# Performance work log

Measured on AMD Instinct MI355X. Metric: run time of the kernel, lower is better.

The kernel has to match this reference:

```python
import jax, jax.numpy as jnp
import numpy as np

N_NODES = 100000
N_EDGES = 600000
N_GRAPHS = 2000
H = 128
L = 3
EPS = 1e-5


def layer_norm(x, g, b):
    m = jnp.mean(x, axis=-1, keepdims=True)
    v = jnp.mean((x - m) ** 2, axis=-1, keepdims=True)
    return (x - m) / jnp.sqrt(v + EPS) * g + b


def setup_inputs() -> dict:
    key = jax.random.key(0)
    ks = jax.random.split(key, 32)
    s = 0.05
    d = {}
    d['atom_features'] = jax.random.normal(ks[0], (N_NODES, 4), jnp.float32)
    d['edge_index'] = jax.random.randint(ks[1], (2, N_EDGES), 0, N_NODES, jnp.int32)
    d['edge_attr'] = jax.random.uniform(ks[2], (N_EDGES, 1), jnp.float32)
    d['batch'] = jnp.sort(jax.random.randint(ks[3], (N_NODES,), 0, N_GRAPHS, jnp.int32))
    # atom encoder
    d['enc_w'] = jax.random.normal(ks[4], (4, H)) * s
    d['enc_b'] = jnp.zeros((H,))
    d['enc_ln_g'] = jnp.ones((H,))
    d['enc_ln_b'] = jnp.zeros((H,))
    # stacked per-layer MPNN params (L layers)
    d['msg_w1'] = jax.random.normal(ks[5], (L, 2 * H + 1, 2 * H)) * s
    d['msg_b1'] = jnp.zeros((L, 2 * H))
    d['msg_w2'] = jax.random.normal(ks[6], (L, 2 * H, H)) * s
    d['msg_b2'] = jnp.zeros((L, H))
    d['gru_wih'] = jax.random.normal(ks[7], (L, 3 * H, H)) * s
    d['gru_whh'] = jax.random.normal(ks[8], (L, 3 * H, H)) * s
    d['gru_bih'] = jnp.zeros((L, 3 * H))
    d['gru_bhh'] = jnp.zeros((L, 3 * H))
    d['ln_g'] = jnp.ones((L, H))
    d['ln_b'] = jnp.zeros((L, H))
    # readout MLP (dropout is eval-mode identity)
    d['ro_w1'] = jax.random.normal(ks[9], (2 * H, H)) * s
    d['ro_b1'] = jnp.zeros((H,))
    d['ro_w2'] = jax.random.normal(ks[10], (H, H // 2)) * s
    d['ro_b2'] = jnp.zeros((H // 2,))
    d['ro_w3'] = jax.random.normal(ks[11], (H // 2, 113)) * s
    d['ro_b3'] = jnp.zeros((113,))
    return d


def _forward(atom_features, edge_attr, enc_w, enc_b, enc_ln_g, enc_ln_b,
             msg_w1, msg_b1, msg_w2, msg_b2, gru_wih, gru_whh, gru_bih, gru_bhh,
             ln_g, ln_b, ro_w1, ro_b1, ro_w2, ro_b2, ro_w3, ro_b3,
             edge_index, batch):
    n = atom_features.shape[0]
    x = layer_norm(jax.nn.relu(atom_features @ enc_w + enc_b), enc_ln_g, enc_ln_b)
    src, dst = edge_index[0], edge_index[1]
    for l in range(L):
        # gather-concat-MLP messages: [E, 2H+1] -> [E, 2H] -> [E, H]
        m = jnp.concatenate([x[src], x[dst], edge_attr], axis=-1)
        m = jax.nn.relu(m @ msg_w1[l] + msg_b1[l]) @ msg_w2[l] + msg_b2[l]
        aggr = jax.ops.segment_sum(m, dst, num_segments=n)  # index_add
        # GRUCell(input=aggr, hidden=x)
        gi = aggr @ gru_wih[l].T + gru_bih[l]
        gh = x @ gru_whh[l].T + gru_bhh[l]
        i_r, i_z, i_n = jnp.split(gi, 3, axis=-1)
        h_r, h_z, h_n = jnp.split(gh, 3, axis=-1)
        r = jax.nn.sigmoid(i_r + h_r)
        z = jax.nn.sigmoid(i_z + h_z)
        nn_ = jnp.tanh(i_n + r * h_n)
        x_new = (1.0 - z) * nn_ + z * x
        x = layer_norm(x + x_new, ln_g[l], ln_b[l])
    # per-graph mean+max pooling
    ones = jnp.ones((n,), x.dtype)
    counts = jax.ops.segment_sum(ones, batch, num_segments=N_GRAPHS)
    mean_pool = jax.ops.segment_sum(x, batch, num_segments=N_GRAPHS) / jnp.maximum(counts, 1.0)[:, None]
    max_pool = jax.ops.segment_max(x, batch, num_segments=N_GRAPHS)
    g = jnp.concatenate([mean_pool, max_pool], axis=-1)  # [B, 2H]
    h1 = jax.nn.relu(g @ ro_w1 + ro_b1)
    h2 = jax.nn.relu(h1 @ ro_w2 + ro_b2)
    return h2 @ ro_w3 + ro_b3  # [B, 113]


def reference(atom_features, edge_index, edge_attr, batch, enc_w, enc_b, enc_ln_g, enc_ln_b,
              msg_w1, msg_b1, msg_w2, msg_b2, gru_wih, gru_whh, gru_bih, gru_bhh,
              ln_g, ln_b, ro_w1, ro_b1, ro_w2, ro_b2, ro_w3, ro_b3):
    return _forward(atom_features, edge_attr, enc_w, enc_b, enc_ln_g, enc_ln_b,
                    msg_w1, msg_b1, msg_w2, msg_b2, gru_wih, gru_whh, gru_bih, gru_bhh,
                    ln_g, ln_b, ro_w1, ro_b1, ro_w2, ro_b2, ro_w3, ro_b3,
                    edge_index, batch)
```

## Files before the change

kernel.cpp:

```cpp
#include <hip/hip_runtime.h>
#include <hip/hip_bf16.h>
#include <math.h>

#define NN 100000
#define NE_TOT 600000
#define NG 2000
#define HD 128
#define NL 3
#define LN_EPS 1e-5f

typedef __attribute__((ext_vector_type(8))) short short8;
typedef __attribute__((ext_vector_type(4))) float f32x4;

__device__ __forceinline__ unsigned short f2bf(float f){
  union { float f; unsigned int u; } x; x.f = f;
  unsigned int r = (x.u + 0x7FFFu + ((x.u >> 16) & 1u)) >> 16;
  return (unsigned short)r;
}
__device__ __forceinline__ float bf2f(unsigned short u){
  union { unsigned int i; float f; } x; x.i = ((unsigned int)u) << 16; return x.f;
}

__device__ __forceinline__ float wave_sum64(float v){
  #pragma unroll
  for (int o = 32; o > 0; o >>= 1) v += __shfl_xor(v, o, 64);
  return v;
}

__global__ __launch_bounds__(256) void k_zero4(float4* p, int n4){
  int i = blockIdx.x * 256 + threadIdx.x;
  if (i < n4) p[i] = make_float4(0.f, 0.f, 0.f, 0.f);
}

__global__ __launch_bounds__(256) void k_hist(const int* __restrict__ ei, int* __restrict__ cnt){
  int e = blockIdx.x * 256 + threadIdx.x;
  if (e < NE_TOT) atomicAdd(&cnt[ei[NE_TOT + e]], 1);
}

__global__ __launch_bounds__(1024) void k_scan1(const int* __restrict__ cnt,
                                                int* __restrict__ loc,
                                                int* __restrict__ bsum){
  __shared__ int w_s[16];
  int t = threadIdx.x, lane = t & 63, wv = t >> 6;
  int g = blockIdx.x * 1024 + t;
  int v = (g < NN) ? cnt[g] : 0;
  int s = v;
  #pragma unroll
  for (int o = 1; o < 64; o <<= 1){
    int u = __shfl_up(s, o, 64);
    if (lane >= o) s += u;
  }
  if (lane == 63) w_s[wv] = s;
  __syncthreads();
  if (t == 0){
    int run = 0;
    #pragma unroll
    for (int i = 0; i < 16; ++i){ int c = w_s[i]; w_s[i] = run; run += c; }
    bsum[blockIdx.x] = run;
  }
  __syncthreads();
  if (g < NN) loc[g] = s - v + w_s[wv];
}

__global__ __launch_bounds__(128) void k_scan2(const int* __restrict__ bsum,
                                               int* __restrict__ bscan){
  __shared__ int w0_s;
  int t = threadIdx.x, lane = t & 63, wv = t >> 6;
  int v = (t < 98) ? bsum[t] : 0;
  int s = v;
  #pragma unroll
  for (int o = 1; o < 64; o <<= 1){
    int u = __shfl_up(s, o, 64);
    if (lane >= o) s += u;
  }
  if (wv == 0 && lane == 63) w0_s = s;
  __syncthreads();
  if (wv == 1) s += w0_s;
  if (t < 98) bscan[t] = s - v;
}

__global__ __launch_bounds__(1024) void k_scan3(const int* __restrict__ loc,
                                                const int* __restrict__ bscan,
                                                int* __restrict__ cur){
  int g = blockIdx.x * 1024 + threadIdx.x;
  if (g < NN) cur[g] = loc[g] + bscan[blockIdx.x];
}

__global__ __launch_bounds__(256) void k_scatter(const int* __restrict__ ei,
    const float* __restrict__ eattr, int* __restrict__ cur,
    int* __restrict__ srcs, int* __restrict__ dsts, float* __restrict__ attrs){
  int e = blockIdx.x * 256 + threadIdx.x;
  if (e >= NE_TOT) return;
  int d = ei[NE_TOT + e];
  int p = atomicAdd(&cur[d], 1);
  srcs[p] = ei[e];
  dsts[p] = d;
  attrs[p] = eattr[e];
}

#define GW_LPL 102400
#define GW_O2  67584
#define GW_O3  84992
__global__ __launch_bounds__(256) void k_gprep(const float* __restrict__ wih,
                                               const float* __restrict__ whh,
                                               unsigned short* __restrict__ gw){
  int idx = blockIdx.x * 256 + threadIdx.x;
  if (idx >= 2 * 3 * 384 * 128) return;
  int which = (idx >= 3 * 384 * 128);
  int i = which ? idx - 3 * 384 * 128 : idx;
  int l = i / 49152;
  int r = i - l * 49152;
  int j = r >> 7, k = r & 127;
  float v = which ? whh[i] : wih[i];
  size_t o;
  if (!which){
    o = (j < 256) ? ((size_t)l * GW_LPL + (size_t)j * 264 + k)
                  : ((size_t)l * GW_LPL + GW_O2 + (size_t)(j - 256) * 136 + k);
  } else {
    o = (j < 256) ? ((size_t)l * GW_LPL + (size_t)j * 264 + 128 + k)
                  : ((size_t)l * GW_LPL + GW_O3 + (size_t)(j - 256) * 136 + k);
  }
  gw[o] = f2bf(v);
}

#define W1N_LS (512 * 136)
__global__ __launch_bounds__(256) void k_mprep(const float* __restrict__ w1,
                                               unsigned short* __restrict__ w1n){
  int idx = blockIdx.x * 256 + threadIdx.x;
  if (idx >= 3 * 512 * 128) return;
  int l = idx / (512 * 128);
  int r = idx - l * (512 * 128);
  int j = r >> 7, k = r & 127;
  const float* wl = w1 + (size_t)l * 257 * 256;
  float v = (j < 256) ? wl[k * 256 + j] : wl[(128 + k) * 256 + (j - 256)];
  w1n[(size_t)l * W1N_LS + j * 136 + k] = f2bf(v);
}

#define W2T_LS (128 * 264)
__global__ __launch_bounds__(256) void k_w2prep(const float* __restrict__ w2,
                                                unsigned short* __restrict__ w2T){
  int idx = blockIdx.x * 256 + threadIdx.x;
  if (idx >= 3 * 128 * 256) return;
  int l = idx >> 15;
  int r = idx & 32767;
  int c = r >> 8, k = r & 255;
  w2T[(size_t)l * W2T_LS + c * 264 + k] = f2bf(w2[(size_t)l * 256 * 128 + k * 128 + c]);
}

__global__ __launch_bounds__(256) void k_enc(const float* __restrict__ af,
    const float* __restrict__ w, const float* __restrict__ b,
    const float* __restrict__ lg, const float* __restrict__ lb,
    unsigned short* __restrict__ xbf){
  int wv = threadIdx.x >> 6, lane = threadIdx.x & 63;
  int n = blockIdx.x * 4 + wv;
  float4 a = *reinterpret_cast<const float4*>(af + (size_t)n * 4);
  int c0 = lane, c1 = lane + 64;
  float v0 = fmaf(a.x, w[c0], fmaf(a.y, w[128 + c0], fmaf(a.z, w[256 + c0], fmaf(a.w, w[384 + c0], b[c0]))));
  float v1 = fmaf(a.x, w[c1], fmaf(a.y, w[128 + c1], fmaf(a.z, w[256 + c1], fmaf(a.w, w[384 + c1], b[c1]))));
  v0 = fmaxf(v0, 0.f); v1 = fmaxf(v1, 0.f);
  float m = wave_sum64(v0 + v1) * (1.f / 128.f);
  float d0 = v0 - m, d1 = v1 - m;
  float var = wave_sum64(d0 * d0 + d1 * d1) * (1.f / 128.f);
  float rstd = rsqrtf(var + LN_EPS);
  xbf[(size_t)n * HD + c0] = f2bf(d0 * rstd * lg[c0] + lb[c0]);
  xbf[(size_t)n * HD + c1] = f2bf(d1 * rstd * lg[c1] + lb[c1]);
}

__global__ __launch_bounds__(256, 2) void k_ngemm(const unsigned short* __restrict__ xbf,
    const unsigned short* __restrict__ w1n, const float* __restrict__ b1,
    unsigned short* __restrict__ gsd){
  int tid = threadIdx.x, lane = tid & 63, wv = tid >> 6;
  int r16 = lane & 15, kg = lane >> 4;
  int n = blockIdx.x * 64 + wv * 16 + r16;
  int nc = (n < NN) ? n : NN - 1;
  short8 bfr[4];
  #pragma unroll
  for (int k0 = 0; k0 < 4; ++k0)
    bfr[k0] = *reinterpret_cast<const short8*>(xbf + (size_t)nc * HD + k0 * 32 + kg * 8);
  f32x4 acc[32];
  #pragma unroll
  for (int it = 0; it < 32; ++it) acc[it] = (f32x4){0.f, 0.f, 0.f, 0.f};
  #pragma unroll
  for (int it = 0; it < 32; ++it){
    const unsigned short* ap = w1n + (size_t)(it * 16 + r16) * 136 + kg * 8;
    #pragma unroll
    for (int k0 = 0; k0 < 4; ++k0){
      short8 af = *reinterpret_cast<const short8*>(ap + k0 * 32);
      acc[it] = __builtin_amdgcn_mfma_f32_16x16x32_bf16(af, bfr[k0], acc[it], 0, 0, 0);
    }
  }
  if (n < NN){
    #pragma unroll
    for (int it = 0; it < 32; ++it){
      int c0 = it * 16 + kg * 4;
      ushort4 h;
      float v0 = acc[it][0], v1 = acc[it][1], v2 = acc[it][2], v3 = acc[it][3];
      if (c0 >= 256){
        v0 += b1[c0 - 256]; v1 += b1[c0 - 255]; v2 += b1[c0 - 254]; v3 += b1[c0 - 253];
      }
      h.x = f2bf(v0); h.y = f2bf(v1); h.z = f2bf(v2); h.w = f2bf(v3);
      *reinterpret_cast<ushort4*>(gsd + (size_t)n * 512 + c0) = h;
    }
  }
}

#define EBM 64
__global__ __launch_bounds__(256, 4) void k_msg(const unsigned short* __restrict__ gsd,
    const int* __restrict__ srcs, const int* __restrict__ dsts,
    const float* __restrict__ attrs, const float* __restrict__ w1attr,
    const unsigned short* __restrict__ w2T, const float* __restrict__ b2,
    float* __restrict__ aggr){
  __shared__ __align__(16) unsigned char smem[33280];
  unsigned short* h_s = (unsigned short*)smem;
  float* scr = (float*)smem;
  __shared__ float w1a_s[256];
  __shared__ float b2_s[128];
  __shared__ int   dst_s[EBM];
  __shared__ float attr_s[EBM];
  int tid = threadIdx.x;
  int lane = tid & 63, wv = tid >> 6;
  int r16 = lane & 15, kg = lane >> 4;
  int ebase = blockIdx.x * EBM;

  w1a_s[tid] = w1attr[tid & 255];
  if (tid < 128) b2_s[tid] = b2[tid];
  if (tid < EBM){ dst_s[tid] = dsts[ebase + tid]; attr_s[tid] = attrs[ebase + tid]; }
  __syncthreads();

  {
    int e = tid >> 2, q = tid & 3;
    int sn = srcs[ebase + e];
    int dn = dst_s[e];
    float at = attr_s[e];
    const unsigned short* gp = gsd + (size_t)sn * 512;
    const unsigned short* dp = gsd + (size_t)dn * 512 + 256;
    #pragma unroll
    for (int j8 = 0; j8 < 8; ++j8){
      int colb = j8 * 32 + q * 8;
      short8 gv = *reinterpret_cast<const short8*>(gp + colb);
      short8 dv = *reinterpret_cast<const short8*>(dp + colb);
      unsigned short hh[8];
      #pragma unroll
      for (int i = 0; i < 8; ++i){
        float v = bf2f((unsigned short)gv[i]) + bf2f((unsigned short)dv[i]) + at * w1a_s[colb + i];
        hh[i] = f2bf(fmaxf(v, 0.f));
      }
      int slot = colb >> 3;
      int slotw = (slot & ~7) | ((slot ^ e) & 7);
      *reinterpret_cast<int4*>(&h_s[e * 256 + slotw * 8]) = *reinterpret_cast<int4*>(hh);
    }
  }
  __syncthreads();

  f32x4 acc2[4][2];
  #pragma unroll
  for (int rt = 0; rt < 4; ++rt)
    #pragma unroll
    for (int ct = 0; ct < 2; ++ct)
      acc2[rt][ct] = (f32x4){0.f, 0.f, 0.f, 0.f};
  int cbase2 = wv * 32;
  {
    short8 a[4], bb[2];
    const unsigned short* w2b = w2T + (size_t)(cbase2 + r16) * 264 + kg * 8;
    for (int k0 = 0; k0 < 8; ++k0){
      #pragma unroll
      for (int rt = 0; rt < 4; ++rt){
        int row = rt * 16 + r16;
        int slot = k0 * 4 + kg;
        int slotw = (slot & ~7) | ((slot ^ row) & 7);
        a[rt] = *reinterpret_cast<const short8*>(&h_s[row * 256 + slotw * 8]);
      }
      #pragma unroll
      for (int ct = 0; ct < 2; ++ct)
        bb[ct] = *reinterpret_cast<const short8*>(w2b + ct * 16 * 264 + k0 * 32);
      #pragma unroll
      for (int rt = 0; rt < 4; ++rt)
        #pragma unroll
        for (int ct = 0; ct < 2; ++ct)
          acc2[rt][ct] = __builtin_amdgcn_mfma_f32_16x16x32_bf16(a[rt], bb[ct], acc2[rt][ct], 0, 0, 0);
    }
  }
  __syncthreads();

  #pragma unroll
  for (int ct = 0; ct < 2; ++ct){
    int col = cbase2 + ct * 16 + r16;
    #pragma unroll
    for (int rt = 0; rt < 4; ++rt){
      #pragma unroll
      for (int r = 0; r < 4; ++r){
        int row = rt * 16 + kg * 4 + r;
        scr[row * 130 + col] = acc2[rt][ct][r];
      }
    }
  }
  __syncthreads();

  {
    int c = tid & 127, h = tid >> 7;
    int r0 = h * 32;
    float bias = b2_s[c];
    int pd = dst_s[r0];
    float acc = scr[r0 * 130 + c] + bias;
    #pragma unroll 4
    for (int r = 1; r < 32; ++r){
      int row = r0 + r;
      float v = scr[row * 130 + c] + bias;
      int d = dst_s[row];
      if (d != pd){
        atomicAdd(&aggr[(size_t)pd * HD + c], acc);
        acc = v; pd = d;
      } else {
        acc += v;
      }
    }
    atomicAdd(&aggr[(size_t)pd * HD + c], acc);
  }
}

#define GRB 64
__global__ __launch_bounds__(256, 2) void k_gru(unsigned short* __restrict__ xbf,
    const float* __restrict__ aggr,
    const unsigned short* __restrict__ gw,
    const float* __restrict__ bih, const float* __restrict__ bhh,
    const float* __restrict__ lg, const float* __restrict__ lb){
  __shared__ unsigned short a_s[GRB * 256];
  int tid = threadIdx.x;
  int lane = tid & 63, wv = tid >> 6;
  int r16 = lane & 15, kg = lane >> 4;
  int nbase = blockIdx.x * GRB;

  {
    int row = tid >> 2, qc = (tid & 3) * 32;
    int n = nbase + row; if (n >= NN) n = NN - 1;
    const float* ap = aggr + (size_t)n * HD + qc;
    #pragma unroll
    for (int j = 0; j < 8; ++j){
      float4 v = *reinterpret_cast<const float4*>(ap + j * 4);
      ushort4 h;
      h.x = f2bf(v.x); h.y = f2bf(v.y); h.z = f2bf(v.z); h.w = f2bf(v.w);
      int col = qc + j * 4;
      int slot = col >> 3;
      int slotw = (slot & ~7) | ((slot ^ row) & 7);
      *reinterpret_cast<ushort4*>(&a_s[row * 256 + slotw * 8 + (col & 7)]) = h;
    }
  }
  {
    int row = tid >> 2, q = tid & 3;
    int n = nbase + row; if (n >= NN) n = NN - 1;
    const unsigned short* xp = xbf + (size_t)n * HD + q * 32;
    #pragma unroll
    for (int j = 0; j < 4; ++j){
      int4 v = *reinterpret_cast<const int4*>(xp + j * 8);
      int col = 128 + q * 32 + j * 8;
      int slot = col >> 3;
      int slotw = (slot & ~7) | ((slot ^ row) & 7);
      *reinterpret_cast<int4*>(&a_s[row * 256 + slotw * 8]) = v;
    }
  }
  __syncthreads();

  int arow = wv * 16 + r16;
  short8 a[8];
  #pragma unroll
  for (int k0 = 0; k0 < 8; ++k0){
    int slot = k0 * 4 + kg;
    int slotw = (slot & ~7) | ((slot ^ arow) & 7);
    a[k0] = *reinterpret_cast<const short8*>(&a_s[arow * 256 + slotw * 8]);
  }

  f32x4 acc1[16], accI[8], accH[8];
  #pragma unroll
  for (int ct = 0; ct < 16; ++ct) acc1[ct] = (f32x4){0.f, 0.f, 0.f, 0.f};
  #pragma unroll
  for (int ct = 0; ct < 8; ++ct){ accI[ct] = (f32x4){0.f, 0.f, 0.f, 0.f}; accH[ct] = (f32x4){0.f, 0.f, 0.f, 0.f}; }

  #pragma unroll
  for (int ct = 0; ct < 16; ++ct){
    const unsigned short* bp = gw + (size_t)(ct * 16 + r16) * 264 + kg * 8;
    #pragma unroll
    for (int k0 = 0; k0 < 8; ++k0){
      short8 b = *reinterpret_cast<const short8*>(bp + k0 * 32);
      acc1[ct] = __builtin_amdgcn_mfma_f32_16x16x32_bf16(a[k0], b, acc1[ct], 0, 0, 0);
    }
  }
  #pragma unroll
  for (int ct = 0; ct < 8; ++ct){
    const unsigned short* bp = gw + GW_O2 + (size_t)(ct * 16 + r16) * 136 + kg * 8;
    #pragma unroll
    for (int k0 = 0; k0 < 4; ++k0){
      short8 b = *reinterpret_cast<const short8*>(bp + k0 * 32);
      accI[ct] = __builtin_amdgcn_mfma_f32_16x16x32_bf16(a[k0], b, accI[ct], 0, 0, 0);
    }
  }
  #pragma unroll
  for (int ct = 0; ct < 8; ++ct){
    const unsigned short* bp = gw + GW_O3 + (size_t)(ct * 16 + r16) * 136 + kg * 8;
    #pragma unroll
    for (int k0 = 0; k0 < 4; ++k0){
      short8 b = *reinterpret_cast<const short8*>(bp + k0 * 32);
      accH[ct] = __builtin_amdgcn_mfma_f32_16x16x32_bf16(a[k0 + 4], b, accH[ct], 0, 0, 0);
    }
  }

  float pre[8][4];
  #pragma unroll
  for (int ct = 0; ct < 8; ++ct){
    int j = ct * 16 + r16;
    float br = bih[j] + bhh[j];
    float bz = bih[j + 128] + bhh[j + 128];
    float bin = bih[j + 256], bhn = bhh[j + 256];
    #pragma unroll
    for (int r = 0; r < 4; ++r){
      int n = nbase + wv * 16 + kg * 4 + r;
      int nc = (n < NN) ? n : NN - 1;
      float xv = bf2f(xbf[(size_t)nc * HD + j]);
      float rg = acc1[ct][r] + br;       rg = 1.f / (1.f + __expf(-rg));
      float zg = acc1[ct + 8][r] + bz;   zg = 1.f / (1.f + __expf(-zg));
      float ng = tanhf(accI[ct][r] + bin + rg * (accH[ct][r] + bhn));
      pre[ct][r] = xv + (1.f - zg) * ng + zg * xv;
    }
  }

  #pragma unroll
  for (int r = 0; r < 4; ++r){
    float s = 0.f;
    #pragma unroll
    for (int ct = 0; ct < 8; ++ct) s += pre[ct][r];
    #pragma unroll
    for (int o = 1; o <= 8; o <<= 1) s += __shfl_xor(s, o, 64);
    float m = s * (1.f / 128.f);
    float v = 0.f;
    #pragma unroll
    for (int ct = 0; ct < 8; ++ct){ float d = pre[ct][r] - m; v += d * d; }
    #pragma unroll
    for (int o = 1; o <= 8; o <<= 1) v += __shfl_xor(v, o, 64);
    float rstd = rsqrtf(v * (1.f / 128.f) + LN_EPS);
    int n = nbase + wv * 16 + kg * 4 + r;
    if (n < NN){
      #pragma unroll
      for (int ct = 0; ct < 8; ++ct){
        int j = ct * 16 + r16;
        xbf[(size_t)n * HD + j] = f2bf((pre[ct][r] - m) * rstd * lg[j] + lb[j]);
      }
    }
  }
}

__device__ __forceinline__ int lowerb(const int* __restrict__ a, int v){
  int lo = 0, hi = NN;
  while (lo < hi){ int mid = (lo + hi) >> 1; if (a[mid] < v) lo = mid + 1; else hi = mid; }
  return lo;
}

__global__ __launch_bounds__(128) void k_pool(const unsigned short* __restrict__ xbf,
    const int* __restrict__ batch,
    const float* __restrict__ w1, const float* __restrict__ b1,
    const float* __restrict__ w2, const float* __restrict__ b2,
    const float* __restrict__ w3, const float* __restrict__ b3,
    float* __restrict__ out){
  __shared__ float g_s[256];
  __shared__ float h1_s[128];
  __shared__ float h2_s[64];
  int g = blockIdx.x, tid = threadIdx.x;
  int s = lowerb(batch, g), t = lowerb(batch, g + 1);
  float sum = 0.f, mx = -INFINITY;
  for (int n = s; n < t; ++n){
    float v = bf2f(xbf[(size_t)n * HD + tid]);
    sum += v; mx = fmaxf(mx, v);
  }
  int cnt = t - s;
  g_s[tid]       = sum / fmaxf((float)cnt, 1.f);
  g_s[tid + 128] = (cnt > 0) ? mx : -INFINITY;
  __syncthreads();
  float a1 = b1[tid];
  for (int k = 0; k < 256; ++k) a1 = fmaf(g_s[k], w1[k * 128 + tid], a1);
  h1_s[tid] = fmaxf(a1, 0.f);
  __syncthreads();
  if (tid < 64){
    float a2 = b2[tid];
    for (int k = 0; k < 128; ++k) a2 = fmaf(h1_s[k], w2[k * 64 + tid], a2);
    h2_s[tid] = fmaxf(a2, 0.f);
  }
  __syncthreads();
  if (tid < 113){
    float a3 = b3[tid];
    for (int k = 0; k < 64; ++k) a3 = fmaf(h2_s[k], w3[k * 113 + tid], a3);
    out[(size_t)g * 113 + tid] = a3;
  }
}

extern "C" void kernel_launch(void* const* d_in, const int* in_sizes, int n_in,
                              void* d_out, int out_size, void* d_ws, size_t ws_size,
                              hipStream_t stream){
  (void)in_sizes; (void)n_in; (void)out_size; (void)ws_size;
  const float* af     = (const float*)d_in[0];
  const int*   ei     = (const int*)  d_in[1];
  const float* eattr  = (const float*)d_in[2];
  const int*   batch  = (const int*)  d_in[3];
  const float* enc_w  = (const float*)d_in[4];
  const float* enc_b  = (const float*)d_in[5];
  const float* enc_lg = (const float*)d_in[6];
  const float* enc_lb = (const float*)d_in[7];
  const float* mw1    = (const float*)d_in[8];
  const float* mb1    = (const float*)d_in[9];
  const float* mw2    = (const float*)d_in[10];
  const float* mb2    = (const float*)d_in[11];
  const float* gwih   = (const float*)d_in[12];
  const float* gwhh   = (const float*)d_in[13];
  const float* gbih   = (const float*)d_in[14];
  const float* gbhh   = (const float*)d_in[15];
  const float* lng    = (const float*)d_in[16];
  const float* lnb    = (const float*)d_in[17];
  const float* rw1    = (const float*)d_in[18];
  const float* rb1    = (const float*)d_in[19];
  const float* rw2    = (const float*)d_in[20];
  const float* rb2    = (const float*)d_in[21];
  const float* rw3    = (const float*)d_in[22];
  const float* rb3    = (const float*)d_in[23];
  float* out = (float*)d_out;
  char* ws = (char*)d_ws;

  size_t off = 0;
  auto carve = [&](size_t bytes)->char*{
    char* p = ws + off;
    off = (off + bytes + 255) & ~(size_t)255;
    return p;
  };
  unsigned short* xbf  = (unsigned short*)carve((size_t)NN * HD * 2);
  float*          aggr = (float*)         carve((size_t)NN * HD * 4);
  unsigned short* gsd  = (unsigned short*)carve((size_t)NN * 512 * 2);
  unsigned short* gw   = (unsigned short*)carve((size_t)3 * GW_LPL * 2);
  unsigned short* w1n  = (unsigned short*)carve((size_t)3 * W1N_LS * 2);
  unsigned short* w2T  = (unsigned short*)carve((size_t)3 * W2T_LS * 2);
  int*   cnt   = (int*)  carve((size_t)NN * 4);
  int*   cur   = (int*)  carve((size_t)NN * 4);
  int*   loc   = (int*)  carve((size_t)NN * 4);
  int*   bsum  = (int*)  carve((size_t)128 * 4);
  int*   bscan = (int*)  carve((size_t)128 * 4);
  int*   srcs  = (int*)  carve((size_t)NE_TOT * 4);
  int*   dsts  = (int*)  carve((size_t)NE_TOT * 4);
  float* attrs = (float*)carve((size_t)NE_TOT * 4);

  k_zero4<<<(NN / 4 + 255) / 256, 256, 0, stream>>>((float4*)cnt, NN / 4);
  k_hist<<<(NE_TOT + 255) / 256, 256, 0, stream>>>(ei, cnt);
  k_scan1<<<98, 1024, 0, stream>>>(cnt, loc, bsum);
  k_scan2<<<1, 128, 0, stream>>>(bsum, bscan);
  k_scan3<<<98, 1024, 0, stream>>>(loc, bscan, cur);
  k_scatter<<<(NE_TOT + 255) / 256, 256, 0, stream>>>(ei, eattr, cur, srcs, dsts, attrs);
  k_gprep<<<1152, 256, 0, stream>>>(gwih, gwhh, gw);
  k_mprep<<<768, 256, 0, stream>>>(mw1, w1n);
  k_w2prep<<<384, 256, 0, stream>>>(mw2, w2T);
  k_enc<<<NN / 4, 256, 0, stream>>>(af, enc_w, enc_b, enc_lg, enc_lb, xbf);

  for (int l = 0; l < NL; ++l){
    k_zero4<<<(NN * HD / 4 + 255) / 256, 256, 0, stream>>>((float4*)aggr, NN * HD / 4);
    k_ngemm<<<(NN + 63) / 64, 256, 0, stream>>>(xbf,
        w1n + (size_t)l * W1N_LS, mb1 + (size_t)l * 256, gsd);
    k_msg<<<NE_TOT / EBM, 256, 0, stream>>>(gsd, srcs, dsts, attrs,
        mw1 + (size_t)l * 257 * 256 + 256 * 256,
        w2T + (size_t)l * W2T_LS, mb2 + (size_t)l * 128, aggr);
    k_gru<<<(NN + GRB - 1) / GRB, 256, 0, stream>>>(xbf, aggr,
        gw + (size_t)l * GW_LPL,
        gbih + (size_t)l * 384, gbhh + (size_t)l * 384,
        lng + (size_t)l * HD, lnb + (size_t)l * HD);
  }
  k_pool<<<NG, 128, 0, stream>>>(xbf, batch, rw1, rb1, rw2, rb2, rw3, rb3, out);
}
```

Before: 1.052 ms.

## Retile GRU kernel for weight reuse and fuse aggr zeroing into ngemm

Each GRU wave now computes a 32-row by 64-column tile, so every loaded weight fragment is used by two MFMA row tiles. The LayerNorm row statistics are combined across the two column-group waves through shared memory, using a one-pass sum and sum-of-squares. The per-layer zeroing of the aggregation buffer moves into the node GEMM kernel, which removes a separate launch. The one-pass variance is slightly less numerically accurate, and the change adds a block barrier.

```diff
diff --git a/kernel.cpp b/kernel.cpp
--- a/kernel.cpp
+++ b/kernel.cpp
@@ -168,9 +168,15 @@
 
 __global__ __launch_bounds__(256, 2) void k_ngemm(const unsigned short* __restrict__ xbf,
     const unsigned short* __restrict__ w1n, const float* __restrict__ b1,
-    unsigned short* __restrict__ gsd){
+    unsigned short* __restrict__ gsd, float* __restrict__ aggr){
   int tid = threadIdx.x, lane = tid & 63, wv = tid >> 6;
   int r16 = lane & 15, kg = lane >> 4;
+  {
+    int nrow = NN - blockIdx.x * 64; if (nrow > 64) nrow = 64;
+    float4* az = (float4*)(aggr + (size_t)blockIdx.x * 64 * HD);
+    int n4 = nrow * (HD / 4);
+    for (int i = tid; i < n4; i += 256) az[i] = make_float4(0.f, 0.f, 0.f, 0.f);
+  }
   int n = blockIdx.x * 64 + wv * 16 + r16;
   int nc = (n < NN) ? n : NN - 1;
   short8 bfr[4];
@@ -325,9 +331,11 @@
     const float* __restrict__ bih, const float* __restrict__ bhh,
     const float* __restrict__ lg, const float* __restrict__ lb){
   __shared__ unsigned short a_s[GRB * 256];
+  __shared__ float psum[GRB][2][2];
   int tid = threadIdx.x;
   int lane = tid & 63, wv = tid >> 6;
   int r16 = lane & 15, kg = lane >> 4;
+  int rg = wv >> 1, cg = wv & 1;
   int nbase = blockIdx.x * GRB;
 
   {
@@ -360,88 +368,112 @@
   }
   __syncthreads();
 
-  int arow = wv * 16 + r16;
-  short8 a[8];
-  #pragma unroll
-  for (int k0 = 0; k0 < 8; ++k0){
-    int slot = k0 * 4 + kg;
-    int slotw = (slot & ~7) | ((slot ^ arow) & 7);
-    a[k0] = *reinterpret_cast<const short8*>(&a_s[arow * 256 + slotw * 8]);
-  }
-
-  f32x4 acc1[16], accI[8], accH[8];
-  #pragma unroll
-  for (int ct = 0; ct < 16; ++ct) acc1[ct] = (f32x4){0.f, 0.f, 0.f, 0.f};
-  #pragma unroll
-  for (int ct = 0; ct < 8; ++ct){ accI[ct] = (f32x4){0.f, 0.f, 0.f, 0.f}; accH[ct] = (f32x4){0.f, 0.f, 0.f, 0.f}; }
-
-  #pragma unroll
-  for (int ct = 0; ct < 16; ++ct){
-    const unsigned short* bp = gw + (size_t)(ct * 16 + r16) * 264 + kg * 8;
+  short8 a[2][8];
+  #pragma unroll
+  for (int rt = 0; rt < 2; ++rt){
+    int arow = rg * 32 + rt * 16 + r16;
     #pragma unroll
     for (int k0 = 0; k0 < 8; ++k0){
-      short8 b = *reinterpret_cast<const short8*>(bp + k0 * 32);
-      acc1[ct] = __builtin_amdgcn_mfma_f32_16x16x32_bf16(a[k0], b, acc1[ct], 0, 0, 0);
-    }
-  }
-  #pragma unroll
-  for (int ct = 0; ct < 8; ++ct){
-    const unsigned short* bp = gw + GW_O2 + (size_t)(ct * 16 + r16) * 136 + kg * 8;
+      int slot = k0 * 4 + kg;
+      int slotw = (slot & ~7) | ((slot ^ arow) & 7);
+      a[rt][k0] = *reinterpret_cast<const short8*>(&a_s[arow * 256 + slotw * 8]);
+    }
+  }
+
+  f32x4 accR[2][4], accZ[2][4], accI[2][4], accH[2][4];
+  #pragma unroll
+  for (int rt = 0; rt < 2; ++rt)
+    #pragma unroll
+    for (int ct = 0; ct < 4; ++ct){
+      accR[rt][ct] = (f32x4){0.f, 0.f, 0.f, 0.f};
+      accZ[rt][ct] = (f32x4){0.f, 0.f, 0.f, 0.f};
+      accI[rt][ct] = (f32x4){0.f, 0.f, 0.f, 0.f};
+      accH[rt][ct] = (f32x4){0.f, 0.f, 0.f, 0.f};
+    }
+
+  int jb = cg * 64;
+  #pragma unroll
+  for (int ct = 0; ct < 4; ++ct){
+    const unsigned short* bpR = gw + (size_t)(jb + ct * 16 + r16) * 264 + kg * 8;
+    const unsigned short* bpZ = gw + (size_t)(128 + jb + ct * 16 + r16) * 264 + kg * 8;
+    #pragma unroll
+    for (int k0 = 0; k0 < 8; ++k0){
+      short8 bR = *reinterpret_cast<const short8*>(bpR + k0 * 32);
+      accR[0][ct] = __builtin_amdgcn_mfma_f32_16x16x32_bf16(a[0][k0], bR, accR[0][ct], 0, 0, 0);
+      accR[1][ct] = __builtin_amdgcn_mfma_f32_16x16x32_bf16(a[1][k0], bR, accR[1][ct], 0, 0, 0);
+      short8 bZ = *reinterpret_cast<const short8*>(bpZ + k0 * 32);
+      accZ[0][ct] = __builtin_amdgcn_mfma_f32_16x16x32_bf16(a[0][k0], bZ, accZ[0][ct], 0, 0, 0);
+      accZ[1][ct] = __builtin_amdgcn_mfma_f32_16x16x32_bf16(a[1][k0], bZ, accZ[1][ct], 0, 0, 0);
+    }
+    const unsigned short* bpI = gw + GW_O2 + (size_t)(jb + ct * 16 + r16) * 136 + kg * 8;
+    const unsigned short* bpH = gw + GW_O3 + (size_t)(jb + ct * 16 + r16) * 136 + kg * 8;
     #pragma unroll
     for (int k0 = 0; k0 < 4; ++k0){
-      short8 b = *reinterpret_cast<const short8*>(bp + k0 * 32);
-      accI[ct] = __builtin_amdgcn_mfma_f32_16x16x32_bf16(a[k0], b, accI[ct], 0, 0, 0);
-    }
-  }
-  #pragma unroll
-  for (int ct = 0; ct < 8; ++ct){
-    const unsigned short* bp = gw + GW_O3 + (size_t)(ct * 16 + r16) * 136 + kg * 8;
-    #pragma unroll
-    for (int k0 = 0; k0 < 4; ++k0){
-      short8 b = *reinterpret_cast<const short8*>(bp + k0 * 32);
-      accH[ct] = __builtin_amdgcn_mfma_f32_16x16x32_bf16(a[k0 + 4], b, accH[ct], 0, 0, 0);
-    }
-  }
-
-  float pre[8][4];
-  #pragma unroll
-  for (int ct = 0; ct < 8; ++ct){
-    int j = ct * 16 + r16;
-    float br = bih[j] + bhh[j];
-    float bz = bih[j + 128] + bhh[j + 128];
-    float bin = bih[j + 256], bhn = bhh[j + 256];
+      short8 bI = *reinterpret_cast<const short8*>(bpI + k0 * 32);
+      accI[0][ct] = __builtin_amdgcn_mfma_f32_16x16x32_bf16(a[0][k0], bI, accI[0][ct], 0, 0, 0);
+      accI[1][ct] = __builtin_amdgcn_mfma_f32_16x16x32_bf16(a[1][k0], bI, accI[1][ct], 0, 0, 0);
+      short8 bH = *reinterpret_cast<const short8*>(bpH + k0 * 32);
+      accH[0][ct] = __builtin_amdgcn_mfma_f32_16x16x32_bf16(a[0][k0 + 4], bH, accH[0][ct], 0, 0, 0);
+      accH[1][ct] = __builtin_amdgcn_mfma_f32_16x16x32_bf16(a[1][k0 + 4], bH, accH[1][ct], 0, 0, 0);
+    }
+  }
+
+  #pragma unroll
+  for (int rt = 0; rt < 2; ++rt){
+    #pragma unroll
+    for (int ct = 0; ct < 4; ++ct){
+      int j = jb + ct * 16 + r16;
+      float br = bih[j] + bhh[j];
+      float bz = bih[j + 128] + bhh[j + 128];
+      float bin = bih[j + 256], bhn = bhh[j + 256];
+      #pragma unroll
+      for (int r = 0; r < 4; ++r){
+        int n = nbase + rg * 32 + rt * 16 + kg * 4 + r;
+        int nc = (n < NN) ? n : NN - 1;
+        float xv = bf2f(xbf[(size_t)nc * HD + j]);
+        float rgt = accR[rt][ct][r] + br;  rgt = 1.f / (1.f + __expf(-rgt));
+        float zg  = accZ[rt][ct][r] + bz;  zg  = 1.f / (1.f + __expf(-zg));
+        float ng  = tanhf(accI[rt][ct][r] + bin + rgt * (accH[rt][ct][r] + bhn));
+        accR[rt][ct][r] = xv + (1.f - zg) * ng + zg * xv;
+      }
+    }
+  }
+
+  #pragma unroll
+  for (int rt = 0; rt < 2; ++rt){
     #pragma unroll
     for (int r = 0; r < 4; ++r){
-      int n = nbase + wv * 16 + kg * 4 + r;
-      int nc = (n < NN) ? n : NN - 1;
-      float xv = bf2f(xbf[(size_t)nc * HD + j]);
-      float rg = acc1[ct][r] + br;       rg = 1.f / (1.f + __expf(-rg));
-      float zg = acc1[ct + 8][r] + bz;   zg = 1.f / (1.f + __expf(-zg));
-      float ng = tanhf(accI[ct][r] + bin + rg * (accH[ct][r] + bhn));
-      pre[ct][r] = xv + (1.f - zg) * ng + zg * xv;
-    }
-  }
-
-  #pragma unroll
-  for (int r = 0; r < 4; ++r){
-    float s = 0.f;
-    #pragma unroll
-    for (int ct = 0; ct < 8; ++ct) s += pre[ct][r];
-    #pragma unroll
-    for (int o = 1; o <= 8; o <<= 1) s += __shfl_xor(s, o, 64);
-    float m = s * (1.f / 128.f);
-    float v = 0.f;
-    #pragma unroll
-    for (int ct = 0; ct < 8; ++ct){ float d = pre[ct][r] - m; v += d * d; }
-    #pragma unroll
-    for (int o = 1; o <= 8; o <<= 1) v += __shfl_xor(v, o, 64);
-    float rstd = rsqrtf(v * (1.f / 128.f) + LN_EPS);
-    int n = nbase + wv * 16 + kg * 4 + r;
-    if (n < NN){
-      #pragma unroll
-      for (int ct = 0; ct < 8; ++ct){
-        int j = ct * 16 + r16;
-        xbf[(size_t)n * HD + j] = f2bf((pre[ct][r] - m) * rstd * lg[j] + lb[j]);
+      float s = 0.f, q = 0.f;
+      #pragma unroll
+      for (int ct = 0; ct < 4; ++ct){ float v = accR[rt][ct][r]; s += v; q += v * v; }
+      #pragma unroll
+      for (int o = 1; o <= 8; o <<= 1){ s += __shfl_xor(s, o, 64); q += __shfl_xor(q, o, 64); }
+      if (r16 == 0){
+        int l = rg * 32 + rt * 16 + kg * 4 + r;
+        psum[l][cg][0] = s;
+        psum[l][cg][1] = q;
+      }
+    }
+  }
+  __syncthreads();
+
+  #pragma unroll
+  for (int rt = 0; rt < 2; ++rt){
+    #pragma unroll
+    for (int r = 0; r < 4; ++r){
+      int l = rg * 32 + rt * 16 + kg * 4 + r;
+      float S = psum[l][0][0] + psum[l][1][0];
+      float Q = psum[l][0][1] + psum[l][1][1];
+      float m = S * (1.f / 128.f);
+      float var = Q * (1.f / 128.f) - m * m;
+      float rstd = rsqrtf(fmaxf(var, 0.f) + LN_EPS);
+      int n = nbase + rg * 32 + rt * 16 + kg * 4 + r;
+      if (n < NN){
+        #pragma unroll
+        for (int ct = 0; ct < 4; ++ct){
+          int j = jb + ct * 16 + r16;
+          xbf[(size_t)n * HD + j] = f2bf((accR[rt][ct][r] - m) * rstd * lg[j] + lb[j]);
+        }
       }
     }
   }
@@ -554,9 +586,8 @@
   k_enc<<<NN / 4, 256, 0, stream>>>(af, enc_w, enc_b, enc_lg, enc_lb, xbf);
 
   for (int l = 0; l < NL; ++l){
-    k_zero4<<<(NN * HD / 4 + 255) / 256, 256, 0, stream>>>((float4*)aggr, NN * HD / 4);
     k_ngemm<<<(NN + 63) / 64, 256, 0, stream>>>(xbf,
-        w1n + (size_t)l * W1N_LS, mb1 + (size_t)l * 256, gsd);
+        w1n + (size_t)l * W1N_LS, mb1 + (size_t)l * 256, gsd, aggr);
     k_msg<<<NE_TOT / EBM, 256, 0, stream>>>(gsd, srcs, dsts, attrs,
         mw1 + (size_t)l * 257 * 256 + 256 * 256,
         w2T + (size_t)l * W2T_LS, mb2 + (size_t)l * 128, aggr);
```

New measurement: 1.008 ms. -4.2%, faster.
